# Optimization experiments

Hardware: AMD Instinct MI355X
Metric: run time of the kernel (lower is better)

Reference implementation:

```python
import jax, jax.numpy as jnp
import numpy as np

H_K, H_V, DK, DV = 8, 16, 128, 128
HIDDEN = 2048
KDIM, VDIM = H_K * DK, H_V * DV          # 1024, 2048
CONV_DIM = 2 * KDIM + VDIM               # 4096
KS = 4                                   # conv kernel size
EPS = 1e-6


def setup_inputs() -> dict:
    key = jax.random.key(0)
    ks = jax.random.split(key, 8)
    B, S = 1, 1024
    return {
        "hidden_states": jax.random.normal(ks[0], (B, S, HIDDEN), jnp.float32),
        "W_qkvz": jax.random.uniform(ks[1], (HIDDEN, 2 * KDIM + 2 * VDIM), jnp.float32, -0.25, 0.25) * 0.1,
        "W_ba": jax.random.uniform(ks[2], (HIDDEN, 2 * H_V), jnp.float32, -0.25, 0.25),
        "conv_w": jax.random.normal(ks[3], (CONV_DIM, KS), jnp.float32) * 0.1,
        "dt_bias": jnp.ones((H_V,), jnp.float32),
        "A_log": jnp.log(jax.random.uniform(ks[4], (H_V,), jnp.float32, 1e-4, 16.0)),
        "norm_weight": jnp.ones((DV,), jnp.float32),
        "W_out": jax.random.uniform(ks[5], (VDIM, HIDDEN), jnp.float32, -0.06, 0.06),
    }


def _split_qkvz_ba(qkvz, ba):
    # mimic fix_query_key_value_ordering: per-k-head interleaved layout
    B, S, _ = qkvz.shape
    vpk = H_V // H_K
    qkvz = qkvz.reshape(B, S, H_K, 2 * DK + 2 * vpk * DV)
    q = qkvz[..., :DK]
    k = qkvz[..., DK:2 * DK]
    v = qkvz[..., 2 * DK:2 * DK + vpk * DV].reshape(B, S, H_V, DV)
    z = qkvz[..., 2 * DK + vpk * DV:].reshape(B, S, H_V, DV)
    ba = ba.reshape(B, S, H_K, 2 * vpk)
    b = ba[..., :vpk].reshape(B, S, H_V)
    a = ba[..., vpk:].reshape(B, S, H_V)
    return q, k, v, z, b, a


def _causal_conv_silu(x, w):
    # x: [B, S, C] ; w: [C, K] depthwise causal conv, then SiLU
    xt = jnp.swapaxes(x, 1, 2)                      # [B, C, S]
    xt = jnp.pad(xt, ((0, 0), (0, 0), (KS - 1, 0)))
    y = jax.lax.conv_general_dilated(
        xt, w[:, None, :], (1,), 'VALID',
        dimension_numbers=('NCH', 'OIH', 'NCH'),
        feature_group_count=w.shape[0])
    return jax.nn.silu(jnp.swapaxes(y, 1, 2))       # [B, S, C]


def _l2norm(x):
    return x * jax.lax.rsqrt(jnp.sum(x * x, axis=-1, keepdims=True) + 1e-6)


def _gated_delta_rule(q, k, v, g, beta):
    # q, k: [B,S,H,DK]; v: [B,S,H,DV]; g, beta: [B,S,H]
    B, S, H, _ = q.shape
    scale = DK ** -0.5
    q = _l2norm(q) * scale
    k = _l2norm(k)
    qs = jnp.moveaxis(q, 1, 0)   # [S,B,H,DK]
    ks = jnp.moveaxis(k, 1, 0)
    vs = jnp.moveaxis(v, 1, 0)
    gs = jnp.moveaxis(g, 1, 0)   # [S,B,H]
    bs = jnp.moveaxis(beta, 1, 0)
    S0 = jnp.zeros((B, H, DK, DV), q.dtype)

    def step(St, xs):
        qt, kt, vt, gt, bt = xs
        St = St * jnp.exp(gt)[..., None, None]
        pred = jnp.einsum('bhk,bhkv->bhv', kt, St)
        delta = (vt - pred) * bt[..., None]
        St = St + jnp.einsum('bhk,bhv->bhkv', kt, delta)
        o = jnp.einsum('bhk,bhkv->bhv', qt, St)
        return St, o

    _, o = jax.lax.scan(step, S0, (qs, ks, vs, gs, bs))
    return jnp.moveaxis(o, 0, 1)  # [B,S,H,DV]


def _gated_rmsnorm(x, z, w):
    # FLA FusedRMSNormGated (silu): rmsnorm(x)*w, gated by silu(z)
    var = jnp.mean(x * x, axis=-1, keepdims=True)
    return (x * jax.lax.rsqrt(var + EPS)) * w * jax.nn.silu(z)


def _forward(hidden_states, W_qkvz, W_ba, conv_w, dt_bias, A_log, norm_weight, W_out):
    B, S, _ = hidden_states.shape
    qkvz = hidden_states @ W_qkvz
    ba = hidden_states @ W_ba
    q, k, v, z, b, a = _split_qkvz_ba(qkvz, ba)
    mixed = jnp.concatenate([q.reshape(B, S, KDIM), k.reshape(B, S, KDIM),
                             v.reshape(B, S, VDIM)], axis=-1)
    mixed = _causal_conv_silu(mixed, conv_w)
    q = mixed[..., :KDIM].reshape(B, S, H_K, DK)
    k = mixed[..., KDIM:2 * KDIM].reshape(B, S, H_K, DK)
    v = mixed[..., 2 * KDIM:].reshape(B, S, H_V, DV)
    beta = jax.nn.sigmoid(b)
    g = -jnp.exp(A_log) * jax.nn.softplus(a + dt_bias)   # [B,S,H_V]
    rep = H_V // H_K
    q = jnp.repeat(q, rep, axis=2)
    k = jnp.repeat(k, rep, axis=2)
    o = _gated_delta_rule(q, k, v, g, beta)              # [B,S,H_V,DV]
    o = _gated_rmsnorm(o, z, norm_weight)
    return o.reshape(B, S, VDIM) @ W_out


def reference(hidden_states, W_qkvz, W_ba, conv_w, dt_bias, A_log, norm_weight, W_out):
    return _forward(hidden_states, W_qkvz, W_ba, conv_w, dt_bias, A_log, norm_weight, W_out)
```

## Files before the change

kernel.cpp:

```cpp
#include <hip/hip_runtime.h>
#include <hip/hip_bf16.h>
#include <math.h>


#define SEQ 1024
#define HID 2048
#define NQKVZ 6144

typedef __attribute__((ext_vector_type(8))) short short8;
typedef __attribute__((ext_vector_type(4))) float f32x4;

__device__ __forceinline__ unsigned short f2bf(float f) {
  __hip_bfloat16 h = __float2bfloat16(f);
  return *reinterpret_cast<unsigned short*>(&h);
}
__device__ __forceinline__ float bf2f(unsigned short u) {
  unsigned int x = ((unsigned int)u) << 16;
  return __int_as_float(x);
}

typedef __attribute__((address_space(3))) void lds_void;
typedef const __attribute__((address_space(1))) void g_void;
__device__ __forceinline__ void gload16(const void* g, void* l) {
  __builtin_amdgcn_global_load_lds((g_void*)g, (lds_void*)l, 16, 0, 0);
}

__global__ __launch_bounds__(256) void cast_bf16(const float* __restrict__ in,
                                                 unsigned short* __restrict__ out,
                                                 int n) {
  const int i = (blockIdx.x * 256 + threadIdx.x) * 4;
  if (i < n) {
    const float4 v = *(const float4*)&in[i];
    ushort4 o;
    o.x = f2bf(v.x); o.y = f2bf(v.y); o.z = f2bf(v.z); o.w = f2bf(v.w);
    *(ushort4*)&out[i] = o;
  }
}

__global__ __launch_bounds__(256) void transpose_cast2(const float* __restrict__ W1,
                                                       unsigned short* __restrict__ W1t,
                                                       const float* __restrict__ W2,
                                                       unsigned short* __restrict__ W2t) {
  __shared__ float tile[64][65];
  int bx = blockIdx.x;
  const float* W;
  unsigned short* Wt;
  int N;
  if (bx < 96) { W = W1; Wt = W1t; N = NQKVZ; }
  else         { W = W2; Wt = W2t; N = HID; bx -= 96; }
  const int n0 = bx * 64, k0 = blockIdx.y * 64;
  const int tc = (threadIdx.x & 15) * 4;
  const int tr = threadIdx.x >> 4;

#pragma unroll
  for (int rr = 0; rr < 64; rr += 16) {
    const float4 v = *(const float4*)&W[(size_t)(k0 + tr + rr) * N + n0 + tc];
    *(float4*)&tile[tr + rr][tc] = v;
  }
  __syncthreads();
#pragma unroll
  for (int rr = 0; rr < 64; rr += 16) {
    const int r = tr + rr;
    ushort4 o;
    o.x = f2bf(tile[tc + 0][r]);
    o.y = f2bf(tile[tc + 1][r]);
    o.z = f2bf(tile[tc + 2][r]);
    o.w = f2bf(tile[tc + 3][r]);
    *(ushort4*)&Wt[(size_t)(n0 + r) * HID + k0 + tc] = o;
  }
}

__global__ __launch_bounds__(256) void transpose_f32(const float* __restrict__ W,
                                                     float* __restrict__ Wt) {
  __shared__ float tile[32][33];
  const int k0 = blockIdx.x * 32;
  const int tx = threadIdx.x & 31, ty = threadIdx.x >> 5;
#pragma unroll
  for (int r = 0; r < 32; r += 8)
    tile[ty + r][tx] = W[(size_t)(k0 + ty + r) * 32 + tx];
  __syncthreads();
#pragma unroll
  for (int r = 0; r < 32; r += 8)
    Wt[(size_t)(ty + r) * HID + k0 + tx] = tile[tx][ty + r];
}

__global__ __launch_bounds__(256) void ba_kernel(const float* __restrict__ X,
                                                 const float* __restrict__ Wbt,
                                                 const float* __restrict__ A_log,
                                                 const float* __restrict__ dt_bias,
                                                 float* __restrict__ gbuf,
                                                 float* __restrict__ bet) {
  const int col = threadIdx.x & 31;
  const int kg  = threadIdx.x >> 5;
  const int s0  = blockIdx.x * 4;
  const float* wp = Wbt + (size_t)col * HID + kg * 256;
  const float* xp = X + (size_t)s0 * HID + kg * 256;

  float a0 = 0.f, a1 = 0.f, a2 = 0.f, a3 = 0.f;
  for (int kk = 0; kk < 256; kk += 4) {
    const float4 w4 = *(const float4*)&wp[kk];
    const float4 x0 = *(const float4*)&xp[kk];
    const float4 x1 = *(const float4*)&xp[kk + HID];
    const float4 x2 = *(const float4*)&xp[kk + 2 * HID];
    const float4 x3 = *(const float4*)&xp[kk + 3 * HID];
    a0 += x0.x * w4.x + x0.y * w4.y + x0.z * w4.z + x0.w * w4.w;
    a1 += x1.x * w4.x + x1.y * w4.y + x1.z * w4.z + x1.w * w4.w;
    a2 += x2.x * w4.x + x2.y * w4.y + x2.z * w4.z + x2.w * w4.w;
    a3 += x3.x * w4.x + x3.y * w4.y + x3.z * w4.z + x3.w * w4.w;
  }
  __shared__ float red[4][32][9];
  red[0][col][kg] = a0;
  red[1][col][kg] = a1;
  red[2][col][kg] = a2;
  red[3][col][kg] = a3;
  __syncthreads();
  if (threadIdx.x < 128) {
    const int r = threadIdx.x >> 5;
    const int c = threadIdx.x & 31;
    float acc = 0.f;
#pragma unroll
    for (int g = 0; g < 8; ++g) acc += red[r][c][g];
    const int s = s0 + r;
    const int hk = c >> 2, j = c & 3;
    if (j < 2) {
      bet[s * 16 + hk * 2 + j] = 1.f / (1.f + expf(-acc));
    } else {
      const int vh = hk * 2 + (j - 2);
      const float x = acc + dt_bias[vh];
      const float sp = (x > 20.f) ? x : log1pf(expf(x));
      gbuf[s * 16 + vh] = -expf(A_log[vh]) * sp;
    }
  }
}

#define SWZ(row) ((KF == 1) ? (((row) >> 1) & 3) : ((row) & 7))

template <int MF, int NF, int KF>
__global__ __launch_bounds__(256) void gemm_bf16(const unsigned short* __restrict__ A,
                                                 const unsigned short* __restrict__ Bt,
                                                 float* __restrict__ C,
                                                 int M, int N, int K) {
  constexpr int BM = 32 * MF, BN = 32 * NF, BK = 32 * KF;
  constexpr int RB  = BK * 2;
  constexpr int APW = (BM * KF / 16) / 4;
  constexpr int BPW = (BN * KF / 16) / 4;
  constexpr int RPG = 16 / KF;
  __shared__ unsigned short As[2][BM * BK];
  __shared__ unsigned short Bs[2][BN * BK];

  const int tid  = threadIdx.x;
  const int lane = tid & 63;
  const int w    = tid >> 6;
  const int wm   = w >> 1, wn = w & 1;
  const int row0 = blockIdx.y * BM, col0 = blockIdx.x * BN;

  const int lrow  = (KF == 1) ? (lane >> 2) : (lane >> 3);
  const int lslot = lane & (4 * KF - 1);
  const int arow  = lane & 15;

  f32x4 acc[MF][NF];
#pragma unroll
  for (int m = 0; m < MF; ++m)
#pragma unroll
    for (int n = 0; n < NF; ++n) acc[m][n] = (f32x4){0.f, 0.f, 0.f, 0.f};

  auto stage = [&](int bi, int kt) {
    const int ko = kt * BK;
#pragma unroll
    for (int u = 0; u < APW; ++u) {
      const int gu = w * APW + u;
      const int row = gu * RPG + lrow;
      const int sg = lslot ^ SWZ(row);
      gload16(A + (size_t)(row0 + row) * K + ko + sg * 8,
              (char*)As[bi] + gu * 1024 + lane * 16);
    }
#pragma unroll
    for (int u = 0; u < BPW; ++u) {
      const int gu = w * BPW + u;
      const int row = gu * RPG + lrow;
      const int sg = lslot ^ SWZ(row);
      gload16(Bt + (size_t)(col0 + row) * K + ko + sg * 8,
              (char*)Bs[bi] + gu * 1024 + lane * 16);
    }
  };

  stage(0, 0);
  __syncthreads();

  int cur = 0;
  const int nk = K / BK;
  for (int kt = 0; kt < nk; ++kt) {
    if (kt + 1 < nk) stage(cur ^ 1, kt + 1);

    const char* asb = (const char*)As[cur];
    const char* bsb = (const char*)Bs[cur];
    short8 af[MF][KF], bf[NF][KF];
#pragma unroll
    for (int m = 0; m < MF; ++m)
#pragma unroll
      for (int kk = 0; kk < KF; ++kk) {
        const int row = wm * (16 * MF) + m * 16 + arow;
        const int slot = kk * 4 + (lane >> 4);
        af[m][kk] = *(const short8*)(asb + row * RB + ((slot ^ SWZ(row)) * 16));
      }
#pragma unroll
    for (int n = 0; n < NF; ++n)
#pragma unroll
      for (int kk = 0; kk < KF; ++kk) {
        const int row = wn * (16 * NF) + n * 16 + arow;
        const int slot = kk * 4 + (lane >> 4);
        bf[n][kk] = *(const short8*)(bsb + row * RB + ((slot ^ SWZ(row)) * 16));
      }
#pragma unroll
    for (int m = 0; m < MF; ++m)
#pragma unroll
      for (int n = 0; n < NF; ++n)
#pragma unroll
        for (int kk = 0; kk < KF; ++kk)
          acc[m][n] = __builtin_amdgcn_mfma_f32_16x16x32_bf16(af[m][kk], bf[n][kk],
                                                              acc[m][n], 0, 0, 0);

    __syncthreads();
    cur ^= 1;
  }

#pragma unroll
  for (int m = 0; m < MF; ++m)
#pragma unroll
    for (int n = 0; n < NF; ++n) {
      const int r0 = row0 + wm * (16 * MF) + m * 16 + (lane >> 4) * 4;
      const int c  = col0 + wn * (16 * NF) + n * 16 + (lane & 15);
#pragma unroll
      for (int r = 0; r < 4; ++r)
        C[(size_t)(r0 + r) * N + c] = acc[m][n][r];
    }
}

#define NT 512
__global__ __launch_bounds__(NT) void chunk_prep(
    const float* __restrict__ qkvz, const float* __restrict__ conv_w,
    const float* __restrict__ gbuf, const float* __restrict__ bet,
    unsigned short* __restrict__ Tg, unsigned short* __restrict__ Gg,
    unsigned short* __restrict__ Wtg, unsigned short* __restrict__ Qtg,
    unsigned short* __restrict__ Khg, float* __restrict__ bvg,
    float* __restrict__ esg) {
  const int h  = blockIdx.x >> 4;
  const int c  = blockIdx.x & 15;
  const int hk = h >> 1;
  const int tid = threadIdx.x;
  const int lane = tid & 63;
  const int w    = tid >> 6;
  const int lr   = lane & 15;
  const int lk   = lane >> 4;

  __shared__ float raw[67][128];
  __shared__ unsigned short Kb[64 * 128];
  __shared__ unsigned short Qb[64 * 128];
  __shared__ unsigned short Bm[64][64];
  __shared__ float cg[64];
  __shared__ float btl[64];

  const int s0 = c * 64;
  const int qcol0 = hk * 768;
  const int kcol0 = hk * 768 + 128;
  const int vcol0 = hk * 768 + 256 + (h & 1) * 128;

  if (tid < 64) {
    float g = gbuf[(s0 + tid) * 16 + h];
#pragma unroll
    for (int d = 1; d < 64; d <<= 1) {
      const float o = __shfl_up(g, d);
      if (tid >= d) g += o;
    }
    cg[tid] = g;
    btl[tid] = bet[(s0 + tid) * 16 + h];
  }

  float4 rq[5], rk[5], rv[5];

#define ISSUE(col0_, rg)                                                      \
  _Pragma("unroll")                                                           \
  for (int ii = 0; ii < 5; ++ii) {                                            \
    const int idx = tid + NT * ii;                                            \
    if (idx < 67 * 32) {                                                      \
      const int r = idx >> 5, cq = (idx & 31) * 4;                            \
      const int sr = s0 - 3 + r;                                              \
      if (sr >= 0)                                                            \
        rg[ii] = *(const float4*)&qkvz[(size_t)sr * NQKVZ + (col0_) + cq];    \
      else { rg[ii].x = 0.f; rg[ii].y = 0.f; rg[ii].z = 0.f; rg[ii].w = 0.f; }\
    }                                                                         \
  }

#define WRITE(rg)                                                             \
  _Pragma("unroll")                                                           \
  for (int ii = 0; ii < 5; ++ii) {                                            \
    const int idx = tid + NT * ii;                                            \
    if (idx < 67 * 32) {                                                      \
      const int r = idx >> 5, cq = (idx & 31) * 4;                            \
      *(float4*)&raw[r][cq] = rg[ii];                                         \
    }                                                                         \
  }

#define CONV_TO(dst, wbase, isq)                                              \
  for (int n = 0; n < 4; ++n) {                                               \
    const int idx = tid + NT * n;                                             \
    const int row = idx >> 5;                                                 \
    const int col = (idx & 31) * 4;                                           \
    float wgt[4][4];                                                          \
    _Pragma("unroll")                                                         \
    for (int x = 0; x < 4; ++x) {                                             \
      const float4 a = *(const float4*)&conv_w[((wbase) + hk * 128 + col + x) * 4]; \
      wgt[x][0] = a.x; wgt[x][1] = a.y; wgt[x][2] = a.z; wgt[x][3] = a.w;     \
    }                                                                         \
    float4 ac = {0.f, 0.f, 0.f, 0.f};                                         \
    _Pragma("unroll")                                                         \
    for (int j = 0; j < 4; ++j) {                                             \
      const float4 xr = *(const float4*)&raw[row + j][col];                   \
      ac.x = fmaf(wgt[0][j], xr.x, ac.x); ac.y = fmaf(wgt[1][j], xr.y, ac.y); \
      ac.z = fmaf(wgt[2][j], xr.z, ac.z); ac.w = fmaf(wgt[3][j], xr.w, ac.w); \
    }                                                                         \
    float4 y;                                                                 \
    y.x = ac.x / (1.f + __expf(-ac.x)); y.y = ac.y / (1.f + __expf(-ac.y));   \
    y.z = ac.z / (1.f + __expf(-ac.z)); y.w = ac.w / (1.f + __expf(-ac.w));   \
    float ss = y.x * y.x + y.y * y.y + y.z * y.z + y.w * y.w;                 \
    _Pragma("unroll")                                                         \
    for (int m = 1; m <= 16; m <<= 1) ss += __shfl_xor(ss, m);                \
    float sc = rsqrtf(ss + 1e-6f);                                            \
    if (isq) sc *= 0.08838834764831845f;                                      \
    const int boff = row * 256 + ((col * 2) ^ ((row & 7) << 4));              \
    ushort4 o = {f2bf(y.x * sc), f2bf(y.y * sc), f2bf(y.z * sc), f2bf(y.w * sc)}; \
    *(ushort4*)((char*)(dst) + boff) = o;                                     \
  }

  ISSUE(qcol0, rq);
  WRITE(rq);
  __syncthreads();
  ISSUE(kcol0, rk);
  CONV_TO(Qb, 0, true);
  __syncthreads();
  WRITE(rk);
  __syncthreads();
  ISSUE(vcol0, rv);
  CONV_TO(Kb, 1024, false);
  __syncthreads();
  WRITE(rv);

  const bool isK = (w < 4);
  const int w4 = w & 3;
  f32x4 dacc[4];
#pragma unroll
  for (int ct = 0; ct < 4; ++ct) dacc[ct] = (f32x4){0.f, 0.f, 0.f, 0.f};
  {
    const int rowA = 16 * w4 + lr;
    const int swA  = (rowA & 7) << 4;
    const char* Ab = isK ? (const char*)Kb : (const char*)Qb;
#pragma unroll
    for (int ks = 0; ks < 4; ++ks) {
      const int kb = ks * 64 + lk * 16;
      const short8 a = *(const short8*)(Ab + rowA * 256 + (kb ^ swA));
#pragma unroll
      for (int ct = 0; ct < 4; ++ct) {
        const int rowB = ct * 16 + lr;
        const short8 bK = *(const short8*)((char*)Kb + rowB * 256 + (kb ^ ((rowB & 7) << 4)));
        dacc[ct] = __builtin_amdgcn_mfma_f32_16x16x32_bf16(a, bK, dacc[ct], 0, 0, 0);
      }
    }
  }
#pragma unroll
  for (int ct = 0; ct < 4; ++ct) {
#pragma unroll
    for (int r = 0; r < 4; ++r) {
      const int i = 16 * w4 + lk * 4 + r;
      const int j = ct * 16 + lr;
      const float e = __expf(cg[i] - cg[j]);
      if (isK) Bm[i][j] = f2bf((j < i) ? btl[i] * e * dacc[ct][r] : 0.f);
      else     Gg[(size_t)blockIdx.x * 4096 + i * 64 + j] =
                   f2bf((j <= i) ? e * dacc[ct][r] : 0.f);
    }
  }
  __syncthreads();

  const float cglast = cg[63];
  if (w == 0) {
    const int l = lane;
    float Tc[64];
#pragma unroll
    for (int i = 0; i < 64; ++i) {
      float v = (i == l) ? 1.f : 0.f;
#pragma unroll
      for (int j = 0; j < i; ++j) v -= bf2f(Bm[i][j]) * Tc[j];
      Tc[i] = v;
    }
#pragma unroll
    for (int i = 0; i < 64; ++i)
      Tg[(size_t)blockIdx.x * 4096 + i * 64 + l] = f2bf(Tc[i]);
    if (lane == 0) esg[blockIdx.x] = __expf(cglast);
  } else {
    const int t2 = tid - 64;
    for (int idx = t2; idx < 2048; idx += 448) {
      const int i = idx >> 5;
      const int dk = (idx & 31) * 4;
      const int boff = i * 256 + ((dk * 2) ^ ((i & 7) << 4));
      const ushort4 kq = *(const ushort4*)((char*)Kb + boff);
      const ushort4 qq = *(const ushort4*)((char*)Qb + boff);
      const float ei = __expf(cg[i]);
      const float wi = btl[i] * ei;
      ushort4 wo = {f2bf(wi * bf2f(kq.x)), f2bf(wi * bf2f(kq.y)),
                    f2bf(wi * bf2f(kq.z)), f2bf(wi * bf2f(kq.w))};
      ushort4 qo = {f2bf(ei * bf2f(qq.x)), f2bf(ei * bf2f(qq.y)),
                    f2bf(ei * bf2f(qq.z)), f2bf(ei * bf2f(qq.w))};
      *(ushort4*)&Wtg[(size_t)blockIdx.x * 8192 + i * 128 + dk] = wo;
      *(ushort4*)&Qtg[(size_t)blockIdx.x * 8192 + i * 128 + dk] = qo;

      float wv[4][4];
#pragma unroll
      for (int x = 0; x < 4; ++x) {
        const float4 a = *(const float4*)&conv_w[(2048 + h * 128 + dk + x) * 4];
        wv[x][0] = a.x; wv[x][1] = a.y; wv[x][2] = a.z; wv[x][3] = a.w;
      }
      float4 va = {0.f, 0.f, 0.f, 0.f};
#pragma unroll
      for (int j = 0; j < 4; ++j) {
        const float4 xv = *(const float4*)&raw[i + j][dk];
        va.x = fmaf(wv[0][j], xv.x, va.x); va.y = fmaf(wv[1][j], xv.y, va.y);
        va.z = fmaf(wv[2][j], xv.z, va.z); va.w = fmaf(wv[3][j], xv.w, va.w);
      }
      float4 bv4;
      bv4.x = btl[i] * va.x / (1.f + __expf(-va.x));
      bv4.y = btl[i] * va.y / (1.f + __expf(-va.y));
      bv4.z = btl[i] * va.z / (1.f + __expf(-va.z));
      bv4.w = btl[i] * va.w / (1.f + __expf(-va.w));
      *(float4*)&bvg[(size_t)blockIdx.x * 8192 + i * 128 + dk] = bv4;
    }
    for (int lin = t2; lin < 8192; lin += 448) {
      const int dk = lin >> 6, i = lin & 63;
      const unsigned short kraw =
          *(const unsigned short*)((char*)Kb + i * 256 + ((dk * 2) ^ ((i & 7) << 4)));
      Khg[(size_t)blockIdx.x * 8192 + lin] = f2bf(__expf(cglast - cg[i]) * bf2f(kraw));
    }
  }
#undef ISSUE
#undef WRITE
#undef CONV_TO
}
#undef NT

struct SFrags {
  short8 wf[4];
  short8 tf[2];
  short8 qf[4];
  short8 gf[2];
  short8 kh[2][2];
  float  bv[4];
  float  es;
};

__device__ __forceinline__ void sload(SFrags& F,
    const unsigned short* __restrict__ Tg, const unsigned short* __restrict__ Gg,
    const unsigned short* __restrict__ Wtg, const unsigned short* __restrict__ Qtg,
    const unsigned short* __restrict__ Khg, const float* __restrict__ bvg,
    const float* __restrict__ esg,
    size_t base, int w, int lr, int lk, int dv0) {
  const unsigned short* T_  = Tg  + base * 4096;
  const unsigned short* G_  = Gg  + base * 4096;
  const unsigned short* W_  = Wtg + base * 8192;
  const unsigned short* Q_  = Qtg + base * 8192;
  const unsigned short* Kh_ = Khg + base * 8192;
  const float* bv_ = bvg + base * 8192;
#pragma unroll
  for (int ks = 0; ks < 4; ++ks) {
    F.wf[ks] = *(const short8*)(W_ + (16 * w + lr) * 128 + ks * 32 + lk * 8);
    F.qf[ks] = *(const short8*)(Q_ + (16 * w + lr) * 128 + ks * 32 + lk * 8);
  }
#pragma unroll
  for (int ks = 0; ks < 2; ++ks) {
    F.tf[ks]    = *(const short8*)(T_ + (16 * w + lr) * 64 + ks * 32 + lk * 8);
    F.gf[ks]    = *(const short8*)(G_ + (16 * w + lr) * 64 + ks * 32 + lk * 8);
    F.kh[0][ks] = *(const short8*)(Kh_ + (32 * w + lr) * 64 + ks * 32 + lk * 8);
    F.kh[1][ks] = *(const short8*)(Kh_ + (32 * w + 16 + lr) * 64 + ks * 32 + lk * 8);
  }
#pragma unroll
  for (int r = 0; r < 4; ++r)
    F.bv[r] = bv_[(16 * w + lk * 4 + r) * 128 + dv0 + lr];
  F.es = esg[base];
}

__global__ __launch_bounds__(256) void scan_rec(
    const unsigned short* __restrict__ Tg, const unsigned short* __restrict__ Gg,
    const unsigned short* __restrict__ Wtg, const unsigned short* __restrict__ Qtg,
    const unsigned short* __restrict__ Khg, const float* __restrict__ bvg,
    const float* __restrict__ esg, float* __restrict__ obuf) {
  const int h   = blockIdx.x & 15;
  const int dvb = blockIdx.x >> 4;
  const int dv0 = dvb * 16;
  const int tid = threadIdx.x;
  const int lane = tid & 63;
  const int w   = tid >> 6;
  const int lr  = lane & 15;
  const int lk  = lane >> 4;

  __shared__ unsigned short Sb[16][136];
  __shared__ unsigned short Ub[16][72];
  __shared__ unsigned short Db[16][72];

  for (int n = tid; n < 16 * 136 / 2; n += 256) ((unsigned int*)Sb)[n] = 0u;

  f32x4 sacc0 = {0.f, 0.f, 0.f, 0.f};
  f32x4 sacc1 = {0.f, 0.f, 0.f, 0.f};

  SFrags fA, fB;
  sload(fA, Tg, Gg, Wtg, Qtg, Khg, bvg, esg, (size_t)h * 16, w, lr, lk, dv0);
  __syncthreads();

#define SCAN_CHUNK(F, c)                                                      \
  {                                                                           \
    short8 sb[4];                                                             \
    _Pragma("unroll")                                                         \
    for (int ks = 0; ks < 4; ++ks)                                            \
      sb[ks] = *(const short8*)(&Sb[lr][ks * 32 + lk * 8]);                   \
    f32x4 au = {0.f, 0.f, 0.f, 0.f};                                          \
    _Pragma("unroll")                                                         \
    for (int ks = 0; ks < 4; ++ks)                                            \
      au = __builtin_amdgcn_mfma_f32_16x16x32_bf16(F.wf[ks], sb[ks], au, 0, 0, 0); \
    {                                                                         \
      ushort4 pk;                                                             \
      _Pragma("unroll")                                                       \
      for (int r = 0; r < 4; ++r)                                             \
        ((unsigned short*)&pk)[r] = f2bf(F.bv[r] - au[r]);                    \
      *(ushort4*)&Ub[lr][16 * w + lk * 4] = pk;                               \
    }                                                                         \
    __syncthreads();                                                          \
    f32x4 ad = {0.f, 0.f, 0.f, 0.f};                                          \
    _Pragma("unroll")                                                         \
    for (int ks = 0; ks < 2; ++ks) {                                          \
      const short8 ub = *(const short8*)(&Ub[lr][ks * 32 + lk * 8]);          \
      ad = __builtin_amdgcn_mfma_f32_16x16x32_bf16(F.tf[ks], ub, ad, 0, 0, 0); \
    }                                                                         \
    {                                                                         \
      ushort4 pk;                                                             \
      _Pragma("unroll")                                                       \
      for (int r = 0; r < 4; ++r) ((unsigned short*)&pk)[r] = f2bf(ad[r]);    \
      *(ushort4*)&Db[lr][16 * w + lk * 4] = pk;                               \
    }                                                                         \
    __syncthreads();                                                          \
    short8 dbf[2];                                                            \
    _Pragma("unroll")                                                         \
    for (int ks = 0; ks < 2; ++ks)                                            \
      dbf[ks] = *(const short8*)(&Db[lr][ks * 32 + lk * 8]);                  \
    f32x4 ao = {0.f, 0.f, 0.f, 0.f};                                          \
    _Pragma("unroll")                                                         \
    for (int ks = 0; ks < 4; ++ks)                                            \
      ao = __builtin_amdgcn_mfma_f32_16x16x32_bf16(F.qf[ks], sb[ks], ao, 0, 0, 0); \
    _Pragma("unroll")                                                         \
    for (int ks = 0; ks < 2; ++ks)                                            \
      ao = __builtin_amdgcn_mfma_f32_16x16x32_bf16(F.gf[ks], dbf[ks], ao, 0, 0, 0); \
    _Pragma("unroll")                                                         \
    for (int r = 0; r < 4; ++r) {                                             \
      const int i = 16 * w + lk * 4 + r;                                      \
      obuf[((size_t)((c) * 64 + i) * 16 + h) * 128 + dv0 + lr] = ao[r];       \
    }                                                                         \
    sacc0 *= F.es;                                                            \
    sacc1 *= F.es;                                                            \
    _Pragma("unroll")                                                         \
    for (int ks = 0; ks < 2; ++ks) {                                          \
      sacc0 = __builtin_amdgcn_mfma_f32_16x16x32_bf16(F.kh[0][ks], dbf[ks], sacc0, 0, 0, 0); \
      sacc1 = __builtin_amdgcn_mfma_f32_16x16x32_bf16(F.kh[1][ks], dbf[ks], sacc1, 0, 0, 0); \
    }                                                                         \
    {                                                                         \
      ushort4 p0, p1;                                                         \
      _Pragma("unroll")                                                       \
      for (int r = 0; r < 4; ++r) {                                           \
        ((unsigned short*)&p0)[r] = f2bf(sacc0[r]);                           \
        ((unsigned short*)&p1)[r] = f2bf(sacc1[r]);                           \
      }                                                                       \
      *(ushort4*)&Sb[lr][32 * w + lk * 4] = p0;                               \
      *(ushort4*)&Sb[lr][32 * w + 16 + lk * 4] = p1;                          \
    }                                                                         \
    __syncthreads();                                                          \
  }

  for (int c = 0; c < 16; c += 2) {
    const int c1 = (c + 1 < 15) ? c + 1 : 15;
    const int c2 = (c + 2 < 15) ? c + 2 : 15;
    sload(fB, Tg, Gg, Wtg, Qtg, Khg, bvg, esg, (size_t)h * 16 + c1, w, lr, lk, dv0);
    SCAN_CHUNK(fA, c);
    sload(fA, Tg, Gg, Wtg, Qtg, Khg, bvg, esg, (size_t)h * 16 + c2, w, lr, lk, dv0);
    SCAN_CHUNK(fB, c + 1);
  }
#undef SCAN_CHUNK
}

__global__ __launch_bounds__(256) void rmsnorm_kernel(const float* __restrict__ obuf,
                                                      const float* __restrict__ qkvz,
                                                      const float* __restrict__ nw,
                                                      unsigned short* __restrict__ on) {
  const int s    = blockIdx.x;
  const int half = threadIdx.x >> 7;
  const int d    = threadIdx.x & 127;
  __shared__ float red[4];

  for (int it = 0; it < 8; ++it) {
    const int vh = it * 2 + half;
    const float x = obuf[((size_t)s * 16 + vh) * 128 + d];
    float ss = x * x;
#pragma unroll
    for (int m = 1; m < 64; m <<= 1) ss += __shfl_xor(ss, m);
    if ((threadIdx.x & 63) == 0) red[threadIdx.x >> 6] = ss;
    __syncthreads();
    const float tot = red[half * 2] + red[half * 2 + 1];

    const float z = qkvz[(size_t)s * NQKVZ + (vh >> 1) * 768 + 512 + (vh & 1) * 128 + d];
    const float y = x * rsqrtf(tot * (1.f / 128.f) + 1e-6f) * nw[d] *
                    (z / (1.f + expf(-z)));
    on[(size_t)s * 2048 + vh * 128 + d] = f2bf(y);
    __syncthreads();
  }
}

extern "C" void kernel_launch(void* const* d_in, const int* in_sizes, int n_in,
                              void* d_out, int out_size, void* d_ws, size_t ws_size,
                              hipStream_t stream) {
  const float* hid     = (const float*)d_in[0];
  const float* W_qkvz  = (const float*)d_in[1];
  const float* W_ba    = (const float*)d_in[2];
  const float* conv_w  = (const float*)d_in[3];
  const float* dt_bias = (const float*)d_in[4];
  const float* A_log   = (const float*)d_in[5];
  const float* norm_w  = (const float*)d_in[6];
  const float* W_out   = (const float*)d_in[7];
  float* out = (float*)d_out;

  char* ws = (char*)d_ws;
  float* qkvz = (float*)ws;                 ws += (size_t)SEQ * NQKVZ * 4;
  char* region2 = ws;                       ws += (size_t)HID * NQKVZ * 2;
  unsigned short* W1t = (unsigned short*)region2;
  float* obuf = (float*)(region2 + 16777216);
  unsigned short* Xb = (unsigned short*)ws; ws += (size_t)SEQ * HID * 2;
  unsigned short* on_bf = Xb;
  unsigned short* W2t = (unsigned short*)ws; ws += (size_t)HID * HID * 2;
  float* gbuf = (float*)ws;                  ws += (size_t)SEQ * 16 * 4;
  float* bet  = (float*)ws;                  ws += (size_t)SEQ * 16 * 4;
  unsigned short* Tg  = (unsigned short*)ws; ws += (size_t)256 * 4096 * 2;
  unsigned short* Gg  = (unsigned short*)ws; ws += (size_t)256 * 4096 * 2;
  unsigned short* Wtg = (unsigned short*)ws; ws += (size_t)256 * 8192 * 2;
  unsigned short* Qtg = (unsigned short*)ws; ws += (size_t)256 * 8192 * 2;
  unsigned short* Khg = (unsigned short*)ws; ws += (size_t)256 * 8192 * 2;
  float* bvg          = (float*)ws;          ws += (size_t)256 * 8192 * 4;
  float* esg          = (float*)ws;          ws += 256 * 4;
  float* Wbt          = (float*)ws;          ws += (size_t)32 * HID * 4;

  cast_bf16<<<dim3(SEQ * HID / 1024), 256, 0, stream>>>(hid, Xb, SEQ * HID);
  transpose_cast2<<<dim3(128, 32), 256, 0, stream>>>(W_qkvz, W1t, W_out, W2t);
  transpose_f32<<<dim3(HID / 32), 256, 0, stream>>>(W_ba, Wbt);
  ba_kernel<<<dim3(SEQ / 4), 256, 0, stream>>>(hid, Wbt, A_log, dt_bias, gbuf, bet);
  gemm_bf16<2, 4, 2><<<dim3(NQKVZ / 128, SEQ / 64), 256, 0, stream>>>(Xb, W1t, qkvz,
                                                                      SEQ, NQKVZ, HID);
  chunk_prep<<<dim3(256), 512, 0, stream>>>(qkvz, conv_w, gbuf, bet,
                                            Tg, Gg, Wtg, Qtg, Khg, bvg, esg);
  scan_rec<<<dim3(128), 256, 0, stream>>>(Tg, Gg, Wtg, Qtg, Khg, bvg, esg, obuf);
  rmsnorm_kernel<<<dim3(SEQ), 256, 0, stream>>>(obuf, qkvz, norm_w, on_bf);
  gemm_bf16<2, 2, 2><<<dim3(HID / 64, SEQ / 64), 256, 0, stream>>>(on_bf, W2t, out,
                                                                   SEQ, HID, HID);
}
```

Before: 173.5 us.

## Store qkvz projection in bf16 and load all conv inputs up front

The first GEMM now writes its qkvz output as bf16 instead of fp32, which halves that intermediate's write and read traffic in chunk_prep and rmsnorm. chunk_prep keeps three separate padded bf16 LDS buffers for q, k and v, issues all global loads at once, and drops the staged load/write/sync sequence that reused one fp32 raw buffer. The cost is extra rounding on the projection outputs (including z) and more LDS per block, which may lower occupancy.

```diff
diff --git a/kernel.cpp b/kernel.cpp
--- a/kernel.cpp
+++ b/kernel.cpp
@@ -135,10 +135,10 @@
 
 #define SWZ(row) ((KF == 1) ? (((row) >> 1) & 3) : ((row) & 7))
 
-template <int MF, int NF, int KF>
+template <int MF, int NF, int KF, bool OUTBF>
 __global__ __launch_bounds__(256) void gemm_bf16(const unsigned short* __restrict__ A,
                                                  const unsigned short* __restrict__ Bt,
-                                                 float* __restrict__ C,
+                                                 void* __restrict__ Cv,
                                                  int M, int N, int K) {
   constexpr int BM = 32 * MF, BN = 32 * NF, BK = 32 * KF;
   constexpr int RB  = BK * 2;
@@ -231,14 +231,18 @@
       const int r0 = row0 + wm * (16 * MF) + m * 16 + (lane >> 4) * 4;
       const int c  = col0 + wn * (16 * NF) + n * 16 + (lane & 15);
 #pragma unroll
-      for (int r = 0; r < 4; ++r)
-        C[(size_t)(r0 + r) * N + c] = acc[m][n][r];
+      for (int r = 0; r < 4; ++r) {
+        if (OUTBF)
+          ((unsigned short*)Cv)[(size_t)(r0 + r) * N + c] = f2bf(acc[m][n][r]);
+        else
+          ((float*)Cv)[(size_t)(r0 + r) * N + c] = acc[m][n][r];
+      }
     }
 }
 
 #define NT 512
 __global__ __launch_bounds__(NT) void chunk_prep(
-    const float* __restrict__ qkvz, const float* __restrict__ conv_w,
+    const unsigned short* __restrict__ qkvz, const float* __restrict__ conv_w,
     const float* __restrict__ gbuf, const float* __restrict__ bet,
     unsigned short* __restrict__ Tg, unsigned short* __restrict__ Gg,
     unsigned short* __restrict__ Wtg, unsigned short* __restrict__ Qtg,
@@ -253,7 +257,9 @@
   const int lr   = lane & 15;
   const int lk   = lane >> 4;
 
-  __shared__ float raw[67][128];
+  __shared__ unsigned short rawq[67 * 132];
+  __shared__ unsigned short rawk[67 * 132];
+  __shared__ unsigned short rawv[67 * 132];
   __shared__ unsigned short Kb[64 * 128];
   __shared__ unsigned short Qb[64 * 128];
   __shared__ unsigned short Bm[64][64];
@@ -265,6 +271,24 @@
   const int kcol0 = hk * 768 + 128;
   const int vcol0 = hk * 768 + 256 + (h & 1) * 128;
 
+  ushort4 rq[5], rk[5], rv[5];
+#pragma unroll
+  for (int ii = 0; ii < 5; ++ii) {
+    const int idx = tid + NT * ii;
+    if (idx < 67 * 32) {
+      const int r = idx >> 5, cq = (idx & 31) * 4;
+      const int sr = s0 - 3 + r;
+      if (sr >= 0) {
+        rq[ii] = *(const ushort4*)&qkvz[(size_t)sr * NQKVZ + qcol0 + cq];
+        rk[ii] = *(const ushort4*)&qkvz[(size_t)sr * NQKVZ + kcol0 + cq];
+        rv[ii] = *(const ushort4*)&qkvz[(size_t)sr * NQKVZ + vcol0 + cq];
+      } else {
+        rq[ii] = (ushort4){0, 0, 0, 0};
+        rk[ii] = (ushort4){0, 0, 0, 0};
+        rv[ii] = (ushort4){0, 0, 0, 0};
+      }
+    }
+  }
   if (tid < 64) {
     float g = gbuf[(s0 + tid) * 16 + h];
 #pragma unroll
@@ -275,33 +299,19 @@
     cg[tid] = g;
     btl[tid] = bet[(s0 + tid) * 16 + h];
   }
-
-  float4 rq[5], rk[5], rv[5];
-
-#define ISSUE(col0_, rg)                                                      \
-  _Pragma("unroll")                                                           \
-  for (int ii = 0; ii < 5; ++ii) {                                            \
-    const int idx = tid + NT * ii;                                            \
-    if (idx < 67 * 32) {                                                      \
-      const int r = idx >> 5, cq = (idx & 31) * 4;                            \
-      const int sr = s0 - 3 + r;                                              \
-      if (sr >= 0)                                                            \
-        rg[ii] = *(const float4*)&qkvz[(size_t)sr * NQKVZ + (col0_) + cq];    \
-      else { rg[ii].x = 0.f; rg[ii].y = 0.f; rg[ii].z = 0.f; rg[ii].w = 0.f; }\
-    }                                                                         \
-  }
-
-#define WRITE(rg)                                                             \
-  _Pragma("unroll")                                                           \
-  for (int ii = 0; ii < 5; ++ii) {                                            \
-    const int idx = tid + NT * ii;                                            \
-    if (idx < 67 * 32) {                                                      \
-      const int r = idx >> 5, cq = (idx & 31) * 4;                            \
-      *(float4*)&raw[r][cq] = rg[ii];                                         \
-    }                                                                         \
-  }
-
-#define CONV_TO(dst, wbase, isq)                                              \
+#pragma unroll
+  for (int ii = 0; ii < 5; ++ii) {
+    const int idx = tid + NT * ii;
+    if (idx < 67 * 32) {
+      const int r = idx >> 5, cq = (idx & 31) * 4;
+      *(ushort4*)&rawq[r * 132 + cq] = rq[ii];
+      *(ushort4*)&rawk[r * 132 + cq] = rk[ii];
+      *(ushort4*)&rawv[r * 132 + cq] = rv[ii];
+    }
+  }
+  __syncthreads();
+
+#define CONV_TO(dst, rawsrc, wbase, isq)                                      \
   for (int n = 0; n < 4; ++n) {                                               \
     const int idx = tid + NT * n;                                             \
     const int row = idx >> 5;                                                 \
@@ -315,9 +325,11 @@
     float4 ac = {0.f, 0.f, 0.f, 0.f};                                         \
     _Pragma("unroll")                                                         \
     for (int j = 0; j < 4; ++j) {                                             \
-      const float4 xr = *(const float4*)&raw[row + j][col];                   \
-      ac.x = fmaf(wgt[0][j], xr.x, ac.x); ac.y = fmaf(wgt[1][j], xr.y, ac.y); \
-      ac.z = fmaf(wgt[2][j], xr.z, ac.z); ac.w = fmaf(wgt[3][j], xr.w, ac.w); \
+      const ushort4 xr4 = *(const ushort4*)&rawsrc[(row + j) * 132 + col];    \
+      ac.x = fmaf(wgt[0][j], bf2f(xr4.x), ac.x);                              \
+      ac.y = fmaf(wgt[1][j], bf2f(xr4.y), ac.y);                              \
+      ac.z = fmaf(wgt[2][j], bf2f(xr4.z), ac.z);                              \
+      ac.w = fmaf(wgt[3][j], bf2f(xr4.w), ac.w);                              \
     }                                                                         \
     float4 y;                                                                 \
     y.x = ac.x / (1.f + __expf(-ac.x)); y.y = ac.y / (1.f + __expf(-ac.y));   \
@@ -332,18 +344,9 @@
     *(ushort4*)((char*)(dst) + boff) = o;                                     \
   }
 
-  ISSUE(qcol0, rq);
-  WRITE(rq);
-  __syncthreads();
-  ISSUE(kcol0, rk);
-  CONV_TO(Qb, 0, true);
-  __syncthreads();
-  WRITE(rk);
-  __syncthreads();
-  ISSUE(vcol0, rv);
-  CONV_TO(Kb, 1024, false);
-  __syncthreads();
-  WRITE(rv);
+  CONV_TO(Qb, rawq, 0, true);
+  CONV_TO(Kb, rawk, 1024, false);
+  __syncthreads();
 
   const bool isK = (w < 4);
   const int w4 = w & 3;
@@ -421,9 +424,11 @@
       float4 va = {0.f, 0.f, 0.f, 0.f};
 #pragma unroll
       for (int j = 0; j < 4; ++j) {
-        const float4 xv = *(const float4*)&raw[i + j][dk];
-        va.x = fmaf(wv[0][j], xv.x, va.x); va.y = fmaf(wv[1][j], xv.y, va.y);
-        va.z = fmaf(wv[2][j], xv.z, va.z); va.w = fmaf(wv[3][j], xv.w, va.w);
+        const ushort4 xv4 = *(const ushort4*)&rawv[(i + j) * 132 + dk];
+        va.x = fmaf(wv[0][j], bf2f(xv4.x), va.x);
+        va.y = fmaf(wv[1][j], bf2f(xv4.y), va.y);
+        va.z = fmaf(wv[2][j], bf2f(xv4.z), va.z);
+        va.w = fmaf(wv[3][j], bf2f(xv4.w), va.w);
       }
       float4 bv4;
       bv4.x = btl[i] * va.x / (1.f + __expf(-va.x));
@@ -439,8 +444,6 @@
       Khg[(size_t)blockIdx.x * 8192 + lin] = f2bf(__expf(cglast - cg[i]) * bf2f(kraw));
     }
   }
-#undef ISSUE
-#undef WRITE
 #undef CONV_TO
 }
 #undef NT
@@ -591,7 +594,7 @@
 }
 
 __global__ __launch_bounds__(256) void rmsnorm_kernel(const float* __restrict__ obuf,
-                                                      const float* __restrict__ qkvz,
+                                                      const unsigned short* __restrict__ qkvz,
                                                       const float* __restrict__ nw,
                                                       unsigned short* __restrict__ on) {
   const int s    = blockIdx.x;
@@ -609,7 +612,7 @@
     __syncthreads();
     const float tot = red[half * 2] + red[half * 2 + 1];
 
-    const float z = qkvz[(size_t)s * NQKVZ + (vh >> 1) * 768 + 512 + (vh & 1) * 128 + d];
+    const float z = bf2f(qkvz[(size_t)s * NQKVZ + (vh >> 1) * 768 + 512 + (vh & 1) * 128 + d]);
     const float y = x * rsqrtf(tot * (1.f / 128.f) + 1e-6f) * nw[d] *
                     (z / (1.f + expf(-z)));
     on[(size_t)s * 2048 + vh * 128 + d] = f2bf(y);
@@ -631,7 +634,7 @@
   float* out = (float*)d_out;
 
   char* ws = (char*)d_ws;
-  float* qkvz = (float*)ws;                 ws += (size_t)SEQ * NQKVZ * 4;
+  unsigned short* qkvz = (unsigned short*)ws; ws += (size_t)SEQ * NQKVZ * 2;
   char* region2 = ws;                       ws += (size_t)HID * NQKVZ * 2;
   unsigned short* W1t = (unsigned short*)region2;
   float* obuf = (float*)(region2 + 16777216);
@@ -653,12 +656,12 @@
   transpose_cast2<<<dim3(128, 32), 256, 0, stream>>>(W_qkvz, W1t, W_out, W2t);
   transpose_f32<<<dim3(HID / 32), 256, 0, stream>>>(W_ba, Wbt);
   ba_kernel<<<dim3(SEQ / 4), 256, 0, stream>>>(hid, Wbt, A_log, dt_bias, gbuf, bet);
-  gemm_bf16<2, 4, 2><<<dim3(NQKVZ / 128, SEQ / 64), 256, 0, stream>>>(Xb, W1t, qkvz,
-                                                                      SEQ, NQKVZ, HID);
+  gemm_bf16<2, 4, 2, true><<<dim3(NQKVZ / 128, SEQ / 64), 256, 0, stream>>>(
+      Xb, W1t, qkvz, SEQ, NQKVZ, HID);
   chunk_prep<<<dim3(256), 512, 0, stream>>>(qkvz, conv_w, gbuf, bet,
                                             Tg, Gg, Wtg, Qtg, Khg, bvg, esg);
   scan_rec<<<dim3(128), 256, 0, stream>>>(Tg, Gg, Wtg, Qtg, Khg, bvg, esg, obuf);
   rmsnorm_kernel<<<dim3(SEQ), 256, 0, stream>>>(obuf, qkvz, norm_w, on_bf);
-  gemm_bf16<2, 2, 2><<<dim3(HID / 64, SEQ / 64), 256, 0, stream>>>(on_bf, W2t, out,
-                                                                   SEQ, HID, HID);
-}
+  gemm_bf16<2, 2, 2, false><<<dim3(HID / 64, SEQ / 64), 256, 0, stream>>>(
+      on_bf, W2t, out, SEQ, HID, HID);
+}
```

After: 171.2 us. Within noise of the previous version (-1.4%).
